# Kernel tuning notes

Hardware: AMD Instinct MI355X
Metric: run time of the kernel (lower is better)

## Reference

```python
import jax, jax.numpy as jnp
import numpy as np

B, S, D, HD = 16, 2048, 1024, 64  # batch, seq, n_embd, head_dim


def setup_inputs() -> dict:
    key = jax.random.key(0)
    ks = jax.random.split(key, 4)
    std = 1.0 / np.sqrt(D)
    return {
        "x": jax.random.normal(ks[0], (B, S, D), dtype=jnp.float32),
        "Wq": jax.random.normal(ks[1], (D, HD), dtype=jnp.float32) * std,
        "bq": jnp.zeros((HD,), dtype=jnp.float32),
        "Wk": jax.random.normal(ks[2], (D, HD), dtype=jnp.float32) * std,
        "bk": jnp.zeros((HD,), dtype=jnp.float32),
        "Wv": jax.random.normal(ks[3], (D, HD), dtype=jnp.float32) * std,
        "bv": jnp.zeros((HD,), dtype=jnp.float32),
    }


def reference(x, Wq, bq, Wk, bk, Wv, bv):
    q = x @ Wq + bq  # [B,S,HD]
    k = x @ Wk + bk
    v = x @ Wv + bv
    scale = jnp.asarray(HD, x.dtype) ** -0.5
    scores = jnp.einsum("bqd,bkd->bqk", q, k) * scale  # [B,S,S]
    seq = x.shape[1]
    causal = jnp.tril(jnp.ones((seq, seq), dtype=bool))  # True = keep
    scores = jnp.where(causal, scores, jnp.asarray(-jnp.inf, scores.dtype))
    probs = jax.nn.softmax(scores, axis=-1)
    return jnp.einsum("bqk,bkd->bqd", probs, v)  # [B,S,HD]
```

## Files before the change

kernel.cpp:

```cpp
#include <hip/hip_runtime.h>
#include <hip/hip_bf16.h>
#include <math.h>

constexpr int Bsz  = 16;
constexpr int Seq  = 2048;
constexpr int Din  = 1024;
constexpr int Hd   = 64;
constexpr int Rows = Bsz * Seq;

typedef short  short8 __attribute__((ext_vector_type(8)));
typedef float  f32x4  __attribute__((ext_vector_type(4)));

__device__ __forceinline__ short bf16_bits(float f) {
    __hip_bfloat16 h = __float2bfloat16(f);
    return __builtin_bit_cast(short, h);
}

__global__ __launch_bounds__(256) void wt_prep(
    const float* __restrict__ Wq, const float* __restrict__ Wk,
    const float* __restrict__ Wv, short* __restrict__ Wf)
{
    const int u     = blockIdx.x * 256 + threadIdx.x;
    const int chunk = u / 768;
    const int rem   = u - chunk * 768;
    const int f     = rem >> 6;
    const int lane  = rem & 63;
    const int wg    = f >> 2, nt = f & 3;
    const int quad  = lane >> 4, l16 = lane & 15;
    const float* W  = (wg == 0) ? Wq : (wg == 1) ? Wk : Wv;
    const int k0 = chunk * 32 + quad * 8;
    const int n  = nt * 16 + l16;
    short8 v;
    #pragma unroll
    for (int j = 0; j < 8; ++j) v[j] = bf16_bits(W[(size_t)(k0 + j) * Hd + n]);
    *(short8*)(Wf + (size_t)u * 8) = v;
}

__global__ __launch_bounds__(256) void qkv_kernel(
    const float* __restrict__ x,
    const short* __restrict__ Wf,
    const float* __restrict__ bq, const float* __restrict__ bk,
    const float* __restrict__ bv,
    short* __restrict__ Qf, short* __restrict__ Kf, short* __restrict__ Vf)
{
    const int tid  = threadIdx.x;
    const int wave = tid >> 6;
    const int lane = tid & 63;
    const int quad = lane >> 4;
    const int l16  = lane & 15;
    const int bx   = blockIdx.x;
    const int m0   = bx * 64;

    const float* xrow = x + (size_t)(m0 + wave * 16 + l16) * Din + quad * 8;

    f32x4 acc[12] = {};

    #pragma unroll 2
    for (int c = 0; c < 32; ++c) {
        const float4 a0 = *(const float4*)(xrow + c * 32);
        const float4 a1 = *(const float4*)(xrow + c * 32 + 4);
        short8 af;
        af[0] = bf16_bits(a0.x); af[1] = bf16_bits(a0.y);
        af[2] = bf16_bits(a0.z); af[3] = bf16_bits(a0.w);
        af[4] = bf16_bits(a1.x); af[5] = bf16_bits(a1.y);
        af[6] = bf16_bits(a1.z); af[7] = bf16_bits(a1.w);
        const short* wsrc = Wf + (size_t)c * 6144 + lane * 8;
        #pragma unroll
        for (int f = 0; f < 12; ++f) {
            const short8 bb = *(const short8*)(wsrc + f * 512);
            acc[f] = __builtin_amdgcn_mfma_f32_16x16x32_bf16(af, bb, acc[f], 0, 0, 0);
        }
    }

    __shared__ __align__(16) short eS[4][2][16 * 72];
    __shared__ __align__(16) short eV[64 * 80];

    #pragma unroll
    for (int wg = 0; wg < 2; ++wg) {
        const float* bias = wg ? bk : bq;
        #pragma unroll
        for (int nt = 0; nt < 4; ++nt) {
            const float bb = bias[nt * 16 + l16];
            #pragma unroll
            for (int r = 0; r < 4; ++r)
                eS[wave][wg][(quad * 4 + r) * 72 + nt * 16 + l16] =
                    bf16_bits(acc[wg * 4 + nt][r] + bb);
        }
    }
    #pragma unroll
    for (int wg = 0; wg < 2; ++wg) {
        const short8 v0 = *(const short8*)&eS[wave][wg][l16 * 72 + quad * 8];
        const short8 v1 = *(const short8*)&eS[wave][wg][l16 * 72 + 32 + quad * 8];
        if (wg == 0) {
            const size_t tg = (size_t)bx * 4 + wave;
            *(short8*)(Qf + (tg * 2 + 0) * 512 + lane * 8) = v0;
            *(short8*)(Qf + (tg * 2 + 1) * 512 + lane * 8) = v1;
        } else {
            *(short8*)(Kf + (((size_t)bx * 2 + 0) * 4 + wave) * 512 + lane * 8) = v0;
            *(short8*)(Kf + (((size_t)bx * 2 + 1) * 4 + wave) * 512 + lane * 8) = v1;
        }
    }

    #pragma unroll
    for (int nt = 0; nt < 4; ++nt) {
        const float bb = bv[nt * 16 + l16];
        #pragma unroll
        for (int r = 0; r < 4; ++r)
            eV[(nt * 16 + l16) * 80 + wave * 16 + quad * 4 + r] =
                bf16_bits(acc[8 + nt][r] + bb);
    }
    __syncthreads();
    #pragma unroll
    for (int s = 0; s < 2; ++s) {
        const int slot   = tid + s * 256;
        const int lane_s = slot & 63;
        const int u      = slot >> 6;
        const int th     = u >> 2, ntd = u & 3;
        const int q_s    = lane_s >> 4, l_s = lane_s & 15;
        const short8 v = *(const short8*)&eV[(ntd * 16 + l_s) * 80 + th * 32 + q_s * 8];
        *(short8*)(Vf + (((size_t)bx * 2 + th) * 4 + ntd) * 512 + lane_s * 8) = v;
    }
}

__global__ __launch_bounds__(256) void attn_kernel(
    const short* __restrict__ Qf, const short* __restrict__ Kf,
    const short* __restrict__ Vf, float* __restrict__ out)
{
    const int tid  = threadIdx.x;
    const int wave = tid >> 6;
    const int lane = tid & 63;
    const int quad = lane >> 4;
    const int l16  = lane & 15;
    const int b    = blockIdx.y;
    const int bx   = blockIdx.x;
    const int qs   = (bx & 1) ? (127 - (bx >> 1)) : (bx >> 1);
    const int dTile = qs >> 2;
    const int tiles = dTile + 1;
    const int qoff  = (qs & 3) * 16;

    __shared__ __align__(16) unsigned char sm[17408 + 512];
    short* Ps   = (short*)sm;
    float* Obuf = (float*)sm;
    float* mb   = (float*)(sm + 17408);
    float* lb   = mb + 64;

    const size_t tg = (size_t)b * 128 + qs;
    const short8 qf0 = *(const short8*)(Qf + (tg * 2 + 0) * 512 + lane * 8);
    const short8 qf1 = *(const short8*)(Qf + (tg * 2 + 1) * 512 + lane * 8);

    f32x4 o[4] = {};
    float m_run[4], l_run[4];
    #pragma unroll
    for (int r = 0; r < 4; ++r) { m_run[r] = -INFINITY; l_run[r] = 0.0f; }

    const float C = 0.125f * 1.44269504088896340736f;

    for (int kt = wave; kt < tiles; kt += 4) {
        const short* ktile = Kf + (size_t)(b * 32 + kt) * 4096;
        const short* vtile = Vf + (size_t)(b * 32 + kt) * 4096;

        f32x4 s[4] = {};
        #pragma unroll
        for (int nt = 0; nt < 4; ++nt) {
            const short8 kf0 = *(const short8*)(ktile + ((0 * 4 + nt) * 64 + lane) * 8);
            const short8 kf1 = *(const short8*)(ktile + ((1 * 4 + nt) * 64 + lane) * 8);
            s[nt] = __builtin_amdgcn_mfma_f32_16x16x32_bf16(qf0, kf0, s[nt], 0, 0, 0);
            s[nt] = __builtin_amdgcn_mfma_f32_16x16x32_bf16(qf1, kf1, s[nt], 0, 0, 0);
        }

        if (kt == dTile) {
            #pragma unroll
            for (int nt = 0; nt < 4; ++nt) {
                const int kg = nt * 16 + l16;
                #pragma unroll
                for (int r = 0; r < 4; ++r) {
                    const int qg = qoff + quad * 4 + r;
                    s[nt][r] = (kg <= qg) ? s[nt][r] * C : -INFINITY;
                }
            }
        } else {
            #pragma unroll
            for (int nt = 0; nt < 4; ++nt)
                #pragma unroll
                for (int r = 0; r < 4; ++r) s[nt][r] *= C;
        }

        float rm[4];
        #pragma unroll
        for (int r = 0; r < 4; ++r)
            rm[r] = fmaxf(fmaxf(s[0][r], s[1][r]), fmaxf(s[2][r], s[3][r]));
        #pragma unroll
        for (int off = 1; off < 16; off <<= 1)
            #pragma unroll
            for (int r = 0; r < 4; ++r)
                rm[r] = fmaxf(rm[r], __shfl_xor(rm[r], off));

        float alpha[4];
        #pragma unroll
        for (int r = 0; r < 4; ++r) {
            const float mn = fmaxf(m_run[r], rm[r]);
            alpha[r] = exp2f(m_run[r] - mn);
            m_run[r] = mn;
        }

        float rs[4] = {0.f, 0.f, 0.f, 0.f};
        #pragma unroll
        for (int nt = 0; nt < 4; ++nt)
            #pragma unroll
            for (int r = 0; r < 4; ++r) {
                const float p = exp2f(s[nt][r] - m_run[r]);
                s[nt][r] = p;
                rs[r] += p;
            }
        #pragma unroll
        for (int off = 1; off < 16; off <<= 1)
            #pragma unroll
            for (int r = 0; r < 4; ++r)
                rs[r] += __shfl_xor(rs[r], off);
        #pragma unroll
        for (int r = 0; r < 4; ++r) l_run[r] = l_run[r] * alpha[r] + rs[r];

        #pragma unroll
        for (int r = 0; r < 4; ++r) {
            o[0][r] *= alpha[r]; o[1][r] *= alpha[r];
            o[2][r] *= alpha[r]; o[3][r] *= alpha[r];
        }

        #pragma unroll
        for (int nt = 0; nt < 4; ++nt)
            #pragma unroll
            for (int r = 0; r < 4; ++r)
                Ps[wave * 1152 + (quad * 4 + r) * 72 + nt * 16 + l16] = bf16_bits(s[nt][r]);

        const short8 pf0 = *(const short8*)&Ps[wave * 1152 + l16 * 72 + quad * 8];
        const short8 pf1 = *(const short8*)&Ps[wave * 1152 + l16 * 72 + 32 + quad * 8];

        #pragma unroll
        for (int nt = 0; nt < 4; ++nt) {
            const short8 vA = *(const short8*)(vtile + ((0 * 4 + nt) * 64 + lane) * 8);
            const short8 vB = *(const short8*)(vtile + ((1 * 4 + nt) * 64 + lane) * 8);
            o[nt] = __builtin_amdgcn_mfma_f32_16x16x32_bf16(pf0, vA, o[nt], 0, 0, 0);
            o[nt] = __builtin_amdgcn_mfma_f32_16x16x32_bf16(pf1, vB, o[nt], 0, 0, 0);
        }
    }

    if (l16 == 0) {
        #pragma unroll
        for (int r = 0; r < 4; ++r) mb[wave * 16 + quad * 4 + r] = m_run[r];
    }
    __syncthreads();

    float fac[4];
    #pragma unroll
    for (int r = 0; r < 4; ++r) {
        const int row = quad * 4 + r;
        const float mg = fmaxf(fmaxf(mb[row], mb[16 + row]),
                               fmaxf(mb[32 + row], mb[48 + row]));
        fac[r] = exp2f(m_run[r] - mg);
    }
    if (l16 == 0) {
        #pragma unroll
        for (int r = 0; r < 4; ++r) lb[wave * 16 + quad * 4 + r] = l_run[r] * fac[r];
    }
    #pragma unroll
    for (int nt = 0; nt < 4; ++nt)
        #pragma unroll
        for (int r = 0; r < 4; ++r)
            Obuf[wave * 1088 + (quad * 4 + r) * 68 + nt * 16 + l16] = o[nt][r] * fac[r];
    __syncthreads();

    {
        const int row = tid >> 4;
        const int c0  = (tid & 15) * 4;
        const float lsum = lb[row] + lb[16 + row] + lb[32 + row] + lb[48 + row];
        float4 a = *(const float4*)&Obuf[0 * 1088 + row * 68 + c0];
        const float4 a1 = *(const float4*)&Obuf[1 * 1088 + row * 68 + c0];
        const float4 a2 = *(const float4*)&Obuf[2 * 1088 + row * 68 + c0];
        const float4 a3 = *(const float4*)&Obuf[3 * 1088 + row * 68 + c0];
        a.x += a1.x + a2.x + a3.x;  a.y += a1.y + a2.y + a3.y;
        a.z += a1.z + a2.z + a3.z;  a.w += a1.w + a2.w + a3.w;
        const float inv = 1.0f / lsum;
        float4 r4 = make_float4(a.x * inv, a.y * inv, a.z * inv, a.w * inv);
        *(float4*)(out + ((size_t)b * Seq + qs * 16 + row) * Hd + c0) = r4;
    }
}

extern "C" void kernel_launch(void* const* d_in, const int* in_sizes, int n_in,
                              void* d_out, int out_size, void* d_ws, size_t ws_size,
                              hipStream_t stream)
{
    const float* x  = (const float*)d_in[0];
    const float* Wq = (const float*)d_in[1];
    const float* bq = (const float*)d_in[2];
    const float* Wk = (const float*)d_in[3];
    const float* bk = (const float*)d_in[4];
    const float* Wv = (const float*)d_in[5];
    const float* bv = (const float*)d_in[6];
    float* out = (float*)d_out;

    short* Qf = (short*)d_ws;
    short* Kf = Qf + (size_t)Rows * Hd;
    short* Vf = Kf + (size_t)Rows * Hd;
    short* Wf = Vf + (size_t)Rows * Hd;

    wt_prep<<<96, 256, 0, stream>>>(Wq, Wk, Wv, Wf);
    qkv_kernel<<<512, 256, 0, stream>>>(x, Wf, bq, bk, bv, Qf, Kf, Vf);
    attn_kernel<<<dim3(128, 16), 256, 0, stream>>>(Qf, Kf, Vf, out);
}
```

Before: 291.3 us.

## Split QKV projection K-dimension across waves with shared-memory reduction

The QKV projection kernel now uses 512-thread blocks that each handle 32 rows instead of 64. The 1024-wide reduction is split into four K-chunks, one per wave pair, and the partial accumulators are combined in LDS with a two-level tree. This doubles the grid and quadruples the wave count per row tile, which adds parallelism and memory-level concurrency for the x streaming. The cost is extra LDS traffic, several block barriers, and only a quarter of the waves doing the epilogue.

```diff
diff --git a/kernel.cpp b/kernel.cpp
--- a/kernel.cpp
+++ b/kernel.cpp
@@ -36,7 +36,7 @@
     *(short8*)(Wf + (size_t)u * 8) = v;
 }
 
-__global__ __launch_bounds__(256) void qkv_kernel(
+__global__ __launch_bounds__(512, 4) void qkv_kernel(
     const float* __restrict__ x,
     const short* __restrict__ Wf,
     const float* __restrict__ bq, const float* __restrict__ bk,
@@ -48,15 +48,17 @@
     const int lane = tid & 63;
     const int quad = lane >> 4;
     const int l16  = lane & 15;
+    const int rg   = wave & 1;
+    const int kh   = wave >> 1;
     const int bx   = blockIdx.x;
-    const int m0   = bx * 64;
-
-    const float* xrow = x + (size_t)(m0 + wave * 16 + l16) * Din + quad * 8;
+
+    const float* xrow = x + (size_t)(bx * 32 + rg * 16 + l16) * Din + quad * 8;
 
     f32x4 acc[12] = {};
 
+    const int c0 = kh * 8;
     #pragma unroll 2
-    for (int c = 0; c < 32; ++c) {
+    for (int c = c0; c < c0 + 8; ++c) {
         const float4 a0 = *(const float4*)(xrow + c * 32);
         const float4 a1 = *(const float4*)(xrow + c * 32 + 4);
         short8 af;
@@ -72,53 +74,86 @@
         }
     }
 
-    __shared__ __align__(16) short eS[4][2][16 * 72];
-    __shared__ __align__(16) short eV[64 * 80];
-
-    #pragma unroll
-    for (int wg = 0; wg < 2; ++wg) {
-        const float* bias = wg ? bk : bq;
+    __shared__ __align__(16) unsigned char smem[49152];
+    float* M  = (float*)smem;
+    short* eS = (short*)smem;
+    short* eV = (short*)(smem + 2 * 2 * 1152 * 2);
+
+    if (kh == 1 || kh == 3) {
+        const int slot = (kh == 1) ? 0 : 1;
+        float* dst = M + (size_t)((slot * 2 + rg) * 12) * 256 + lane * 4;
+        #pragma unroll
+        for (int f = 0; f < 12; ++f) *(f32x4*)(dst + f * 256) = acc[f];
+    }
+    __syncthreads();
+    if (kh == 0 || kh == 2) {
+        const int slot = (kh == 0) ? 0 : 1;
+        const float* src = M + (size_t)((slot * 2 + rg) * 12) * 256 + lane * 4;
+        #pragma unroll
+        for (int f = 0; f < 12; ++f) acc[f] += *(const f32x4*)(src + f * 256);
+    }
+    __syncthreads();
+    if (kh == 2) {
+        float* dst = M + (size_t)(rg * 12) * 256 + lane * 4;
+        #pragma unroll
+        for (int f = 0; f < 12; ++f) *(f32x4*)(dst + f * 256) = acc[f];
+    }
+    __syncthreads();
+    if (kh == 0) {
+        const float* src = M + (size_t)(rg * 12) * 256 + lane * 4;
+        #pragma unroll
+        for (int f = 0; f < 12; ++f) acc[f] += *(const f32x4*)(src + f * 256);
+    }
+    __syncthreads();
+
+    if (kh == 0) {
+        #pragma unroll
+        for (int wg = 0; wg < 2; ++wg) {
+            const float* bias = wg ? bk : bq;
+            short* strip = eS + (size_t)(rg * 2 + wg) * 1152;
+            #pragma unroll
+            for (int nt = 0; nt < 4; ++nt) {
+                const float bb = bias[nt * 16 + l16];
+                #pragma unroll
+                for (int r = 0; r < 4; ++r)
+                    strip[(quad * 4 + r) * 72 + nt * 16 + l16] =
+                        bf16_bits(acc[wg * 4 + nt][r] + bb);
+            }
+        }
+        #pragma unroll
+        for (int wg = 0; wg < 2; ++wg) {
+            const short* strip = eS + (size_t)(rg * 2 + wg) * 1152;
+            const short8 v0 = *(const short8*)&strip[l16 * 72 + quad * 8];
+            const short8 v1 = *(const short8*)&strip[l16 * 72 + 32 + quad * 8];
+            if (wg == 0) {
+                const size_t tg = (size_t)bx * 2 + rg;
+                *(short8*)(Qf + (tg * 2 + 0) * 512 + lane * 8) = v0;
+                *(short8*)(Qf + (tg * 2 + 1) * 512 + lane * 8) = v1;
+            } else {
+                const size_t t64 = bx >> 1;
+                const int ntK = (bx & 1) * 2 + rg;
+                *(short8*)(Kf + ((t64 * 2 + 0) * 4 + ntK) * 512 + lane * 8) = v0;
+                *(short8*)(Kf + ((t64 * 2 + 1) * 4 + ntK) * 512 + lane * 8) = v1;
+            }
+        }
         #pragma unroll
         for (int nt = 0; nt < 4; ++nt) {
-            const float bb = bias[nt * 16 + l16];
+            const float bb = bv[nt * 16 + l16];
             #pragma unroll
             for (int r = 0; r < 4; ++r)
-                eS[wave][wg][(quad * 4 + r) * 72 + nt * 16 + l16] =
-                    bf16_bits(acc[wg * 4 + nt][r] + bb);
-        }
-    }
-    #pragma unroll
-    for (int wg = 0; wg < 2; ++wg) {
-        const short8 v0 = *(const short8*)&eS[wave][wg][l16 * 72 + quad * 8];
-        const short8 v1 = *(const short8*)&eS[wave][wg][l16 * 72 + 32 + quad * 8];
-        if (wg == 0) {
-            const size_t tg = (size_t)bx * 4 + wave;
-            *(short8*)(Qf + (tg * 2 + 0) * 512 + lane * 8) = v0;
-            *(short8*)(Qf + (tg * 2 + 1) * 512 + lane * 8) = v1;
-        } else {
-            *(short8*)(Kf + (((size_t)bx * 2 + 0) * 4 + wave) * 512 + lane * 8) = v0;
-            *(short8*)(Kf + (((size_t)bx * 2 + 1) * 4 + wave) * 512 + lane * 8) = v1;
-        }
-    }
-
-    #pragma unroll
-    for (int nt = 0; nt < 4; ++nt) {
-        const float bb = bv[nt * 16 + l16];
-        #pragma unroll
-        for (int r = 0; r < 4; ++r)
-            eV[(nt * 16 + l16) * 80 + wave * 16 + quad * 4 + r] =
-                bf16_bits(acc[8 + nt][r] + bb);
-    }
-    __syncthreads();
-    #pragma unroll
-    for (int s = 0; s < 2; ++s) {
-        const int slot   = tid + s * 256;
-        const int lane_s = slot & 63;
-        const int u      = slot >> 6;
-        const int th     = u >> 2, ntd = u & 3;
+                eV[(nt * 16 + l16) * 40 + rg * 16 + quad * 4 + r] =
+                    bf16_bits(acc[8 + nt][r] + bb);
+        }
+    }
+    __syncthreads();
+    if (tid < 256) {
+        const int lane_s = tid & 63;
+        const int ntd    = tid >> 6;
         const int q_s    = lane_s >> 4, l_s = lane_s & 15;
-        const short8 v = *(const short8*)&eV[(ntd * 16 + l_s) * 80 + th * 32 + q_s * 8];
-        *(short8*)(Vf + (((size_t)bx * 2 + th) * 4 + ntd) * 512 + lane_s * 8) = v;
+        const size_t t64 = bx >> 1;
+        const int th     = bx & 1;
+        const short8 v = *(const short8*)&eV[(ntd * 16 + l_s) * 40 + q_s * 8];
+        *(short8*)(Vf + ((t64 * 2 + th) * 4 + ntd) * 512 + lane_s * 8) = v;
     }
 }
 
@@ -304,6 +339,6 @@
     short* Wf = Vf + (size_t)Rows * Hd;
 
     wt_prep<<<96, 256, 0, stream>>>(Wq, Wk, Wv, Wf);
-    qkv_kernel<<<512, 256, 0, stream>>>(x, Wf, bq, bk, bv, Qf, Kf, Vf);
+    qkv_kernel<<<1024, 512, 0, stream>>>(x, Wf, bq, bk, bv, Qf, Kf, Vf);
     attn_kernel<<<dim3(128, 16), 256, 0, stream>>>(Qf, Kf, Vf, out);
 }
```

Result: slower. 304.1 us (+4.4%).
